# Kernel tuning notes

Measured on AMD Instinct MI355X. Metric: run time of the kernel, lower is better.

The kernel has to match this reference:

```python
import jax, jax.numpy as jnp
import numpy as np

N_NODES = 50000
N_EDGES = 1600000
POS_DIM = 64
IN_FEATS = 128
OUT_FEATS = 128
EDGE_MLP_DIM = 32


def setup_inputs() -> dict:
    key = jax.random.key(0)
    ks = jax.random.split(key, 8)
    x = jax.random.normal(ks[0], (N_NODES, POS_DIM + IN_FEATS), dtype=jnp.float32)
    edge_index = jax.random.randint(ks[1], (2, N_EDGES), 0, N_NODES, dtype=jnp.int32)
    # glorot for weight_noformer [in_feats, out_feats]
    stdv = float(np.sqrt(6.0 / (IN_FEATS + OUT_FEATS)))
    w_no = jax.random.uniform(ks[2], (IN_FEATS, OUT_FEATS), dtype=jnp.float32, minval=-stdv, maxval=stdv)
    bias = jnp.zeros((OUT_FEATS,), dtype=jnp.float32)
    # edge MLP: Linear(1, 32) -> Linear(32, 1) -> Sigmoid (no inner activation, faithful to source)
    lim1 = float(np.sqrt(1.0 / 1.0))
    mlp_w1 = jax.random.uniform(ks[3], (1, EDGE_MLP_DIM), dtype=jnp.float32, minval=-lim1, maxval=lim1)
    mlp_b1 = jax.random.uniform(ks[4], (EDGE_MLP_DIM,), dtype=jnp.float32, minval=-lim1, maxval=lim1)
    lim2 = float(np.sqrt(1.0 / EDGE_MLP_DIM))
    mlp_w2 = jax.random.uniform(ks[5], (EDGE_MLP_DIM, 1), dtype=jnp.float32, minval=-lim2, maxval=lim2)
    mlp_b2 = jax.random.uniform(ks[6], (1,), dtype=jnp.float32, minval=-lim2, maxval=lim2)
    return {"x": x, "edge_index": edge_index, "w_no": w_no, "bias": bias,
            "mlp_w1": mlp_w1, "mlp_b1": mlp_b1, "mlp_w2": mlp_w2, "mlp_b2": mlp_b2}


def reference(x, edge_index, w_no, bias, mlp_w1, mlp_b1, mlp_w2, mlp_b2):
    N = x.shape[0]
    coors = x[:, :POS_DIM]            # [N, pos_dim]
    feats = x[:, POS_DIM:]            # [N, in_feats]

    # gcn_norm with added self-loops (improved=False -> fill value 1)
    loop = jnp.arange(N, dtype=edge_index.dtype)
    row = jnp.concatenate([edge_index[0], loop])   # source
    col = jnp.concatenate([edge_index[1], loop])   # target
    ew = jnp.ones(row.shape[0], dtype=x.dtype)
    deg = jax.ops.segment_sum(ew, col, num_segments=N)
    dinv = jnp.where(deg > 0, jax.lax.rsqrt(deg), 0.0)
    ew = dinv[row] * ew * dinv[col]                # [E+N]

    # per-edge squared relative distance in positional space
    rel = coors[row] - coors[col]                  # [E+N, pos_dim]
    rel_dist = jnp.sum(rel * rel, axis=-1, keepdims=True)  # [E+N, 1]

    # tiny edge MLP + sigmoid (Linear -> Linear -> sigmoid)
    h = rel_dist @ mlp_w1 + mlp_b1                 # [E+N, mlp_dim]
    pe = jax.nn.sigmoid(h @ mlp_w2 + mlp_b2)       # [E+N, 1]

    # message = pe * norm_weight * x_j ; scatter-add into target nodes
    msg = pe * ew[:, None] * feats[row]            # [E+N, in_feats]
    m_i = jax.ops.segment_sum(msg, col, num_segments=N)  # [N, in_feats]

    hidden = m_i @ w_no + bias                     # [N, out_feats]
    return jnp.concatenate([coors, hidden], axis=-1)
```

## Files before the change

kernel.cpp:

```cpp
#include <hip/hip_runtime.h>
#include <math.h>

constexpr int NN = 50000;
constexpr int NE = 1600000;
constexpr int PD = 64;
constexpr int XD = 192;

constexpr int NB   = 3125;
constexpr int CAPF = 768;
constexpr int NCB  = 196;
constexpr int CAPC = 10240;
constexpr int RBLK = 782;
constexpr int CH2  = 5;

constexpr int OFF_PV    = 64;
constexpr int OFF_HPRE  = OFF_PV    + 100096;
constexpr int OFF_CCUR  = OFF_HPRE  + 50048;
constexpr int OFF_FCUR  = OFF_CCUR  + 256;
constexpr int OFF_CDATA = OFF_FCUR  + 3136;
constexpr int OFF_BDATA = OFF_CDATA + NCB * CAPC;
constexpr int OFF_CBQ   = OFF_BDATA + NB * CAPF;
constexpr int OFF_FBQ   = OFF_CBQ   + NN * 16;
constexpr int OFF_WBT   = OFF_FBQ   + NN * 32;

typedef __attribute__((ext_vector_type(8))) short bf16x8;
typedef __attribute__((ext_vector_type(4))) float f32x4;
typedef __attribute__((ext_vector_type(2))) float f32x2;

__device__ __forceinline__ unsigned short f2bf(float f) {
    unsigned u = __float_as_uint(f);
    return (unsigned short)((u + 0x7FFFu + ((u >> 16) & 1u)) >> 16);
}

__global__ __launch_bounds__(256) void k_pack(const float* __restrict__ x,
                                              const int* __restrict__ rowv,
                                              const int* __restrict__ colv,
                                              const float* __restrict__ w_no,
                                              const float* __restrict__ w1,
                                              const float* __restrict__ b1,
                                              const float* __restrict__ w2,
                                              const float* __restrict__ b2,
                                              float* __restrict__ out,
                                              unsigned* __restrict__ cbq,
                                              unsigned* __restrict__ fbqu,
                                              unsigned* __restrict__ ccur,
                                              unsigned* __restrict__ cdata,
                                              unsigned short* __restrict__ wbt,
                                              float* __restrict__ pv,
                                              float* __restrict__ AB) {
    __shared__ int hist[NCB];
    __shared__ int pre[NCB];
    __shared__ unsigned gbase[NCB];
    __shared__ int scanbuf[256];
    __shared__ unsigned stag[2048];
    __shared__ unsigned char binof[2048];

    int t = threadIdx.x;
    if (blockIdx.x < RBLK) {
        int base = blockIdx.x * 2048;
        int cnt = NE - base; if (cnt > 2048) cnt = 2048;
        for (int i = t; i < NCB; i += 256) hist[i] = 0;
        __syncthreads();
        unsigned myrec[8]; int mybin[8], myrank[8];
        #pragma unroll
        for (int j = 0; j < 8; ++j) {
            int idx = base + j * 256 + t;
            mybin[j] = -1;
            if (idx < NE) {
                int c = colv[idx], r = rowv[idx];
                int bin = c >> 8;
                mybin[j]  = bin;
                myrank[j] = atomicAdd(&hist[bin], 1);
                myrec[j]  = ((unsigned)c << 16) | (unsigned)r;
            }
        }
        __syncthreads();
        int v = (t < NCB) ? hist[t] : 0;
        scanbuf[t] = v; __syncthreads();
        for (int d = 1; d < 256; d <<= 1) {
            int u = (t >= d) ? scanbuf[t - d] : 0;
            __syncthreads(); scanbuf[t] += u; __syncthreads();
        }
        if (t < NCB) {
            pre[t]   = scanbuf[t] - v;
            gbase[t] = v ? atomicAdd(&ccur[t], (unsigned)v) : 0u;
        }
        __syncthreads();
        #pragma unroll
        for (int j = 0; j < 8; ++j) {
            if (mybin[j] >= 0) {
                int slot = pre[mybin[j]] + myrank[j];
                stag[slot]  = myrec[j];
                binof[slot] = (unsigned char)mybin[j];
            }
        }
        __syncthreads();
        for (int s = t; s < cnt; s += 256) {
            int bin = binof[s];
            unsigned dst = gbase[bin] + (unsigned)(s - pre[bin]);
            if (dst < CAPC)
                cdata[(size_t)bin * CAPC + dst] = stag[s];
        }
        return;
    }

    int tid = (blockIdx.x - RBLK) * 256 + t;
    if (tid < 16384) wbt[tid] = f2bf(w_no[(tid & 127) * 128 + (tid >> 7)]);
    if (tid == 0) {
        float a = 0.f, b = 0.f;
        for (int k = 0; k < 32; ++k) { a += w1[k] * w2[k]; b += b1[k] * w2[k]; }
        AB[0] = a; AB[1] = b + b2[0];
    }
    int wid = tid >> 6, lane = tid & 63;
    if (wid < NN && lane < 48) {
        const float4 v = *(const float4*)&x[(size_t)wid * XD + lane * 4];
        if (lane < 16) {
            *(float4*)&out[(size_t)wid * XD + lane * 4] = v;
            unsigned p = 0;
            p = __builtin_amdgcn_cvt_pk_fp8_f32(v.x, v.y, p, false);
            p = __builtin_amdgcn_cvt_pk_fp8_f32(v.z, v.w, p, true);
            cbq[(size_t)wid * 16 + lane] = p;
            f32x2 lo = __builtin_amdgcn_cvt_pk_f32_fp8(p, false);
            f32x2 hi = __builtin_amdgcn_cvt_pk_f32_fp8(p, true);
            float ssq = lo.x * lo.x + lo.y * lo.y + hi.x * hi.x + hi.y * hi.y;
            #pragma unroll
            for (int o = 8; o >= 1; o >>= 1) ssq += __shfl_xor(ssq, o);
            if (lane == 0) pv[(size_t)wid * 2 + 1] = ssq;
        } else {
            unsigned p = 0;
            p = __builtin_amdgcn_cvt_pk_fp8_f32(v.x, v.y, p, false);
            p = __builtin_amdgcn_cvt_pk_fp8_f32(v.z, v.w, p, true);
            fbqu[(size_t)wid * 32 + (lane - 16)] = p;
        }
    }
}

__global__ __launch_bounds__(256) void k_scat2(const unsigned* __restrict__ ccur,
                                               const unsigned* __restrict__ cdata,
                                               unsigned* __restrict__ fcur,
                                               unsigned* __restrict__ bdata) {
    __shared__ int hist[16];
    __shared__ int pre[16];
    __shared__ unsigned gbase[16];
    __shared__ unsigned stag[2048];
    __shared__ unsigned char binof[2048];

    int cb = blockIdx.x / CH2, k = blockIdx.x % CH2;
    int len = (int)ccur[cb]; if (len > CAPC) len = CAPC;
    int base = k * 2048;
    if (base >= len) return;
    int cnt = len - base; if (cnt > 2048) cnt = 2048;
    int t = threadIdx.x;
    if (t < 16) hist[t] = 0;
    __syncthreads();

    const unsigned* seg = cdata + (size_t)cb * CAPC + base;
    unsigned myrec[8]; int mybin[8], myrank[8];
    #pragma unroll
    for (int j = 0; j < 8; ++j) {
        int idx = j * 256 + t;
        mybin[j] = -1;
        if (idx < cnt) {
            unsigned rec = seg[idx];
            int c = (int)(rec >> 16);
            int bin = (c >> 4) & 15;
            mybin[j]  = bin;
            myrank[j] = atomicAdd(&hist[bin], 1);
            myrec[j]  = ((unsigned)(c & 15) << 16) | (rec & 0xFFFFu);
        }
    }
    __syncthreads();
    if (t == 0) {
        int run = 0;
        for (int i = 0; i < 16; ++i) { pre[i] = run; run += hist[i]; }
    }
    __syncthreads();
    if (t < 16)
        gbase[t] = hist[t] ? atomicAdd(&fcur[cb * 16 + t], (unsigned)hist[t]) : 0u;
    __syncthreads();
    #pragma unroll
    for (int j = 0; j < 8; ++j) {
        if (mybin[j] >= 0) {
            int slot = pre[mybin[j]] + myrank[j];
            stag[slot]  = myrec[j];
            binof[slot] = (unsigned char)mybin[j];
        }
    }
    __syncthreads();
    for (int s = t; s < cnt; s += 256) {
        int bin = binof[s];
        unsigned dst = gbase[bin] + (unsigned)(s - pre[bin]);
        if (dst < CAPF)
            bdata[(size_t)(cb * 16 + bin) * CAPF + dst] = stag[s];
    }
}

__global__ __launch_bounds__(256) void k_deg(const unsigned* __restrict__ fcur,
                                             const unsigned* __restrict__ bdata,
                                             float* __restrict__ pv,
                                             unsigned* __restrict__ hpre) {
    __shared__ int hist[16];
    __shared__ int pre[16];
    int b = blockIdx.x, t = threadIdx.x;
    if (t < 16) hist[t] = 0;
    __syncthreads();

    int cnt = (int)fcur[b]; if (cnt > CAPF) cnt = CAPF;
    const unsigned* seg = bdata + (size_t)b * CAPF;
    for (int g = t; g < cnt; g += 256)
        atomicAdd(&hist[seg[g] >> 16], 1);
    __syncthreads();
    if (t == 0) {
        int run = 0;
        for (int i = 0; i < 16; ++i) { pre[i] = run; run += hist[i]; }
    }
    __syncthreads();
    if (t < 16) {
        int d = b * 16 + t;
        pv[(size_t)d * 2] = rsqrtf((float)hist[t] + 1.0f);
        hpre[d] = ((unsigned)pre[t] << 16) | (unsigned)hist[t];
    }
}

__global__ __launch_bounds__(256) void k_gather(const unsigned* __restrict__ fcur,
                                                const unsigned* __restrict__ bdata,
                                                const unsigned* __restrict__ cbq,
                                                const unsigned char* __restrict__ fbq,
                                                const float* __restrict__ pv,
                                                const unsigned* __restrict__ hpre,
                                                const float* __restrict__ AB,
                                                const float* __restrict__ bias,
                                                const unsigned short* __restrict__ wbt,
                                                float* __restrict__ out) {
    __shared__ unsigned srcL[CAPF + 64];
    __shared__ float    wgtL[CAPF + 64];
    __shared__ uint4    dcq[16][4];
    __shared__ unsigned mLu[16][68];
    __shared__ int preS[16];
    __shared__ int degS[16];
    __shared__ int curL[16];
    __shared__ float dvd[16];
    __shared__ float nsd[16];

    int b = blockIdx.x, t = threadIdx.x;

    if (t < 16) {
        int d = b * 16 + t;
        unsigned hp = hpre[d];
        preS[t] = (int)(hp >> 16);
        degS[t] = (int)(hp & 0xFFFFu);
        curL[t] = (int)(hp >> 16);
        float2 p = *(const float2*)&pv[(size_t)d * 2];
        dvd[t] = p.x;
        nsd[t] = p.y;
    }
    if (t < 64)
        dcq[t >> 2][t & 3] = ((const uint4*)(cbq + (size_t)(b * 16 + (t >> 2)) * 16))[t & 3];
    __syncthreads();

    float A = AB[0], Bc = AB[1];
    float sigB = __builtin_amdgcn_rcpf(1.0f + __expf(-Bc));

    int group = t >> 2, sub = t & 3;
    int cnt = (int)fcur[b]; if (cnt > CAPF) cnt = CAPF;
    const unsigned* seg = bdata + (size_t)b * CAPF;
    #pragma unroll 2
    for (int base = 0; base < cnt; base += 64) {
        int g = base + group;
        bool valid = g < cnt;
        int gc = valid ? g : cnt - 1;
        unsigned rec = seg[gc];
        int d5 = rec >> 16;
        int s  = rec & 0xFFFF;
        float2 ps = *(const float2*)&pv[(size_t)s * 2];
        uint4 sq = ((const uint4*)(cbq + (size_t)s * 16))[sub];
        uint4 dq = dcq[d5][sub];
        f32x2 dots = {0.f, 0.f};
        dots += __builtin_amdgcn_cvt_pk_f32_fp8(sq.x, false) *
                __builtin_amdgcn_cvt_pk_f32_fp8(dq.x, false);
        dots += __builtin_amdgcn_cvt_pk_f32_fp8(sq.x, true) *
                __builtin_amdgcn_cvt_pk_f32_fp8(dq.x, true);
        dots += __builtin_amdgcn_cvt_pk_f32_fp8(sq.y, false) *
                __builtin_amdgcn_cvt_pk_f32_fp8(dq.y, false);
        dots += __builtin_amdgcn_cvt_pk_f32_fp8(sq.y, true) *
                __builtin_amdgcn_cvt_pk_f32_fp8(dq.y, true);
        dots += __builtin_amdgcn_cvt_pk_f32_fp8(sq.z, false) *
                __builtin_amdgcn_cvt_pk_f32_fp8(dq.z, false);
        dots += __builtin_amdgcn_cvt_pk_f32_fp8(sq.z, true) *
                __builtin_amdgcn_cvt_pk_f32_fp8(dq.z, true);
        dots += __builtin_amdgcn_cvt_pk_f32_fp8(sq.w, false) *
                __builtin_amdgcn_cvt_pk_f32_fp8(dq.w, false);
        dots += __builtin_amdgcn_cvt_pk_f32_fp8(sq.w, true) *
                __builtin_amdgcn_cvt_pk_f32_fp8(dq.w, true);
        float sp = dots.x + dots.y;
        sp += __shfl_xor(sp, 1);
        sp += __shfl_xor(sp, 2);
        float ss = ps.y + nsd[d5] - 2.0f * sp;
        float w  = ps.x * dvd[d5] *
                   __builtin_amdgcn_rcpf(1.0f + __expf(-(A * ss + Bc)));
        if (valid && sub == 0) {
            int slot = atomicAdd(&curL[d5], 1);
            srcL[slot] = (unsigned)s;
            wgtL[slot] = w;
        }
    }
    __syncthreads();

    int wl = t >> 6, lane = t & 63;
    int eslot = lane >> 4, dg = lane & 15;

    for (int i = 0; i < 4; ++i) {
        int d5 = wl * 4 + i;
        int d  = b * 16 + d5;

        int deg = degS[d5], s0 = preS[d5];
        float dv = dvd[d5];
        float w0 = (eslot == 0) ? dv * dv * sigB : 0.f;
        f32x2 w02 = {w0, w0};
        uint2 fd = *(const uint2*)(fbq + (size_t)d * 128 + dg * 8);
        f32x2 a01 = w02 * __builtin_amdgcn_cvt_pk_f32_fp8(fd.x, false);
        f32x2 a23 = w02 * __builtin_amdgcn_cvt_pk_f32_fp8(fd.x, true);
        f32x2 a45 = w02 * __builtin_amdgcn_cvt_pk_f32_fp8(fd.y, false);
        f32x2 a67 = w02 * __builtin_amdgcn_cvt_pk_f32_fp8(fd.y, true);

        #pragma unroll 4
        for (int j = 0; j < deg; j += 4) {
            int jj = j + eslot;
            int e  = s0 + ((jj < deg) ? jj : 0);
            float w = (jj < deg) ? wgtL[e] : 0.f;
            int s = (int)srcL[e];
            f32x2 w2 = {w, w};
            uint2 f = *(const uint2*)(fbq + (size_t)s * 128 + dg * 8);
            a01 += w2 * __builtin_amdgcn_cvt_pk_f32_fp8(f.x, false);
            a23 += w2 * __builtin_amdgcn_cvt_pk_f32_fp8(f.x, true);
            a45 += w2 * __builtin_amdgcn_cvt_pk_f32_fp8(f.y, false);
            a67 += w2 * __builtin_amdgcn_cvt_pk_f32_fp8(f.y, true);
        }
        float a0 = a01.x, a1 = a01.y, a2 = a23.x, a3 = a23.y;
        float a4 = a45.x, a5 = a45.y, a6 = a67.x, a7 = a67.y;
        a0 += __shfl_xor(a0, 16); a0 += __shfl_xor(a0, 32);
        a1 += __shfl_xor(a1, 16); a1 += __shfl_xor(a1, 32);
        a2 += __shfl_xor(a2, 16); a2 += __shfl_xor(a2, 32);
        a3 += __shfl_xor(a3, 16); a3 += __shfl_xor(a3, 32);
        a4 += __shfl_xor(a4, 16); a4 += __shfl_xor(a4, 32);
        a5 += __shfl_xor(a5, 16); a5 += __shfl_xor(a5, 32);
        a6 += __shfl_xor(a6, 16); a6 += __shfl_xor(a6, 32);
        a7 += __shfl_xor(a7, 16); a7 += __shfl_xor(a7, 32);

        if (lane < 16) {
            uint4 o;
            o.x = (unsigned)f2bf(a0) | ((unsigned)f2bf(a1) << 16);
            o.y = (unsigned)f2bf(a2) | ((unsigned)f2bf(a3) << 16);
            o.z = (unsigned)f2bf(a4) | ((unsigned)f2bf(a5) << 16);
            o.w = (unsigned)f2bf(a6) | ((unsigned)f2bf(a7) << 16);
            *(uint4*)&mLu[d5][dg * 4] = o;
        }
    }
    __syncthreads();

    {
        int l15 = lane & 15, kg = lane >> 4;
        f32x4 acc[2];
        acc[0] = (f32x4){0.f, 0.f, 0.f, 0.f};
        acc[1] = (f32x4){0.f, 0.f, 0.f, 0.f};
        #pragma unroll
        for (int kk = 0; kk < 4; ++kk) {
            bf16x8 a = *(const bf16x8*)&mLu[l15][kk * 16 + kg * 4];
            #pragma unroll
            for (int nt = 0; nt < 2; ++nt) {
                int col = wl * 32 + nt * 16 + l15;
                bf16x8 bf = *(const bf16x8*)&wbt[(size_t)col * 128 + kk * 32 + kg * 8];
                acc[nt] = __builtin_amdgcn_mfma_f32_16x16x32_bf16(a, bf, acc[nt], 0, 0, 0);
            }
        }
        #pragma unroll
        for (int nt = 0; nt < 2; ++nt) {
            int col = wl * 32 + nt * 16 + l15;
            float bv = bias[col];
            #pragma unroll
            for (int q = 0; q < 4; ++q) {
                int row = kg * 4 + q;
                out[(size_t)(b * 16 + row) * XD + PD + col] = acc[nt][q] + bv;
            }
        }
    }
}

extern "C" void kernel_launch(void* const* d_in, const int* in_sizes, int n_in,
                              void* d_out, int out_size, void* d_ws, size_t ws_size,
                              hipStream_t stream) {
    const float* x    = (const float*)d_in[0];
    const int*   ei   = (const int*)d_in[1];
    const float* w_no = (const float*)d_in[2];
    const float* bias = (const float*)d_in[3];
    const float* w1   = (const float*)d_in[4];
    const float* b1   = (const float*)d_in[5];
    const float* w2   = (const float*)d_in[6];
    const float* b2   = (const float*)d_in[7];
    float* out = (float*)d_out;
    float* ws  = (float*)d_ws;

    float*          AB    = ws;
    float*          pv    = ws + OFF_PV;
    unsigned*       hpre  = (unsigned*)(ws + OFF_HPRE);
    unsigned*       ccur  = (unsigned*)(ws + OFF_CCUR);
    unsigned*       fcur  = (unsigned*)(ws + OFF_FCUR);
    unsigned*       cdata = (unsigned*)(ws + OFF_CDATA);
    unsigned*       bdata = (unsigned*)(ws + OFF_BDATA);
    unsigned*       cbq   = (unsigned*)(ws + OFF_CBQ);
    unsigned*       fbq   = (unsigned*)(ws + OFF_FBQ);
    unsigned short* wbt   = (unsigned short*)(ws + OFF_WBT);

    hipMemsetAsync(ccur, 0, (size_t)(256 + 3136) * sizeof(int), stream);

    k_pack<<<RBLK + 12500, 256, 0, stream>>>(x, ei, ei + NE, w_no, w1, b1, w2, b2,
                                             out, cbq, fbq, ccur, cdata, wbt, pv, AB);
    k_scat2<<<NCB * CH2, 256, 0, stream>>>(ccur, cdata, fcur, bdata);
    k_deg<<<NB, 256, 0, stream>>>(fcur, bdata, pv, hpre);

    k_gather<<<NB, 256, 0, stream>>>(fcur, bdata, cbq, (const unsigned char*)fbq,
                                     pv, hpre, AB, bias, wbt, out);
}
```

Baseline: 113.7 us.

## Split node packing across pack, scatter and degree kernels to fill idle blocks

Node packing (copying coordinates to the output, fp8 quantization of coordinates and features, squared-norm computation) was done entirely in k_pack. It is now divided into three roughly equal node ranges, each handled by extra blocks appended to k_pack, k_scat2 and k_deg. The aim is to run this bandwidth-bound node work alongside the small, latency-bound scatter and degree kernels instead of lengthening the first kernel. The risk is contention with those kernels' memory traffic and extra block scheduling overhead.

Measured after the change: 112.2 us. No clear change (-1.4%).

```diff
diff --git a/kernel.cpp b/kernel.cpp
--- a/kernel.cpp
+++ b/kernel.cpp
@@ -12,6 +12,13 @@
 constexpr int CAPC = 10240;
 constexpr int RBLK = 782;
 constexpr int CH2  = 5;
+constexpr int SBLK = NCB * CH2;
+
+constexpr int NPB1 = 4167;
+constexpr int NPB2 = 4167;
+constexpr int NPB3 = 4166;
+constexpr int NBASE2 = 16668;
+constexpr int NBASE3 = 33336;
 
 constexpr int OFF_PV    = 64;
 constexpr int OFF_HPRE  = OFF_PV    + 100096;
@@ -30,6 +37,34 @@
 __device__ __forceinline__ unsigned short f2bf(float f) {
     unsigned u = __float_as_uint(f);
     return (unsigned short)((u + 0x7FFFu + ((u >> 16) & 1u)) >> 16);
+}
+
+__device__ __forceinline__ void nodepack(int wid, int lane,
+                                         const float* __restrict__ x,
+                                         float* __restrict__ out,
+                                         unsigned* __restrict__ cbq,
+                                         unsigned* __restrict__ fbqu,
+                                         float* __restrict__ pv) {
+    if (wid >= NN || lane >= 48) return;
+    const float4 v = *(const float4*)&x[(size_t)wid * XD + lane * 4];
+    if (lane < 16) {
+        *(float4*)&out[(size_t)wid * XD + lane * 4] = v;
+        unsigned p = 0;
+        p = __builtin_amdgcn_cvt_pk_fp8_f32(v.x, v.y, p, false);
+        p = __builtin_amdgcn_cvt_pk_fp8_f32(v.z, v.w, p, true);
+        cbq[(size_t)wid * 16 + lane] = p;
+        f32x2 lo = __builtin_amdgcn_cvt_pk_f32_fp8(p, false);
+        f32x2 hi = __builtin_amdgcn_cvt_pk_f32_fp8(p, true);
+        float ssq = lo.x * lo.x + lo.y * lo.y + hi.x * hi.x + hi.y * hi.y;
+        #pragma unroll
+        for (int o = 8; o >= 1; o >>= 1) ssq += __shfl_xor(ssq, o);
+        if (lane == 0) pv[(size_t)wid * 2 + 1] = ssq;
+    } else {
+        unsigned p = 0;
+        p = __builtin_amdgcn_cvt_pk_fp8_f32(v.x, v.y, p, false);
+        p = __builtin_amdgcn_cvt_pk_fp8_f32(v.z, v.w, p, true);
+        fbqu[(size_t)wid * 32 + (lane - 16)] = p;
+    }
 }
 
 __global__ __launch_bounds__(256) void k_pack(const float* __restrict__ x,
@@ -104,53 +139,44 @@
         return;
     }
 
-    int tid = (blockIdx.x - RBLK) * 256 + t;
+    int nb = blockIdx.x - RBLK;
+    int tid = nb * 256 + t;
     if (tid < 16384) wbt[tid] = f2bf(w_no[(tid & 127) * 128 + (tid >> 7)]);
     if (tid == 0) {
         float a = 0.f, b = 0.f;
         for (int k = 0; k < 32; ++k) { a += w1[k] * w2[k]; b += b1[k] * w2[k]; }
         AB[0] = a; AB[1] = b + b2[0];
     }
-    int wid = tid >> 6, lane = tid & 63;
-    if (wid < NN && lane < 48) {
-        const float4 v = *(const float4*)&x[(size_t)wid * XD + lane * 4];
-        if (lane < 16) {
-            *(float4*)&out[(size_t)wid * XD + lane * 4] = v;
-            unsigned p = 0;
-            p = __builtin_amdgcn_cvt_pk_fp8_f32(v.x, v.y, p, false);
-            p = __builtin_amdgcn_cvt_pk_fp8_f32(v.z, v.w, p, true);
-            cbq[(size_t)wid * 16 + lane] = p;
-            f32x2 lo = __builtin_amdgcn_cvt_pk_f32_fp8(p, false);
-            f32x2 hi = __builtin_amdgcn_cvt_pk_f32_fp8(p, true);
-            float ssq = lo.x * lo.x + lo.y * lo.y + hi.x * hi.x + hi.y * hi.y;
-            #pragma unroll
-            for (int o = 8; o >= 1; o >>= 1) ssq += __shfl_xor(ssq, o);
-            if (lane == 0) pv[(size_t)wid * 2 + 1] = ssq;
-        } else {
-            unsigned p = 0;
-            p = __builtin_amdgcn_cvt_pk_fp8_f32(v.x, v.y, p, false);
-            p = __builtin_amdgcn_cvt_pk_fp8_f32(v.z, v.w, p, true);
-            fbqu[(size_t)wid * 32 + (lane - 16)] = p;
-        }
-    }
+    nodepack(nb * 4 + (t >> 6), t & 63, x, out, cbq, fbqu, pv);
 }
 
 __global__ __launch_bounds__(256) void k_scat2(const unsigned* __restrict__ ccur,
                                                const unsigned* __restrict__ cdata,
                                                unsigned* __restrict__ fcur,
-                                               unsigned* __restrict__ bdata) {
+                                               unsigned* __restrict__ bdata,
+                                               const float* __restrict__ x,
+                                               float* __restrict__ out,
+                                               unsigned* __restrict__ cbq,
+                                               unsigned* __restrict__ fbqu,
+                                               float* __restrict__ pv) {
     __shared__ int hist[16];
     __shared__ int pre[16];
     __shared__ unsigned gbase[16];
     __shared__ unsigned stag[2048];
     __shared__ unsigned char binof[2048];
 
+    int t = threadIdx.x;
+    if (blockIdx.x >= SBLK) {
+        int nb = blockIdx.x - SBLK;
+        nodepack(NBASE2 + nb * 4 + (t >> 6), t & 63, x, out, cbq, fbqu, pv);
+        return;
+    }
+
     int cb = blockIdx.x / CH2, k = blockIdx.x % CH2;
     int len = (int)ccur[cb]; if (len > CAPC) len = CAPC;
     int base = k * 2048;
     if (base >= len) return;
     int cnt = len - base; if (cnt > 2048) cnt = 2048;
-    int t = threadIdx.x;
     if (t < 16) hist[t] = 0;
     __syncthreads();
 
@@ -198,10 +224,19 @@
 __global__ __launch_bounds__(256) void k_deg(const unsigned* __restrict__ fcur,
                                              const unsigned* __restrict__ bdata,
                                              float* __restrict__ pv,
-                                             unsigned* __restrict__ hpre) {
+                                             unsigned* __restrict__ hpre,
+                                             const float* __restrict__ x,
+                                             float* __restrict__ out,
+                                             unsigned* __restrict__ cbq,
+                                             unsigned* __restrict__ fbqu) {
     __shared__ int hist[16];
     __shared__ int pre[16];
     int b = blockIdx.x, t = threadIdx.x;
+    if (b >= NB) {
+        int nb = b - NB;
+        nodepack(NBASE3 + nb * 4 + (t >> 6), t & 63, x, out, cbq, fbqu, pv);
+        return;
+    }
     if (t < 16) hist[t] = 0;
     __syncthreads();
 
@@ -413,10 +448,12 @@
 
     hipMemsetAsync(ccur, 0, (size_t)(256 + 3136) * sizeof(int), stream);
 
-    k_pack<<<RBLK + 12500, 256, 0, stream>>>(x, ei, ei + NE, w_no, w1, b1, w2, b2,
-                                             out, cbq, fbq, ccur, cdata, wbt, pv, AB);
-    k_scat2<<<NCB * CH2, 256, 0, stream>>>(ccur, cdata, fcur, bdata);
-    k_deg<<<NB, 256, 0, stream>>>(fcur, bdata, pv, hpre);
+    k_pack<<<RBLK + NPB1, 256, 0, stream>>>(x, ei, ei + NE, w_no, w1, b1, w2, b2,
+                                            out, cbq, fbq, ccur, cdata, wbt, pv, AB);
+    k_scat2<<<SBLK + NPB2, 256, 0, stream>>>(ccur, cdata, fcur, bdata,
+                                             x, out, cbq, fbq, pv);
+    k_deg<<<NB + NPB3, 256, 0, stream>>>(fcur, bdata, pv, hpre,
+                                         x, out, cbq, fbq);
 
     k_gather<<<NB, 256, 0, stream>>>(fcur, bdata, cbq, (const unsigned char*)fbq,
                                      pv, hpre, AB, bias, wbt, out);
```
